# Kernel optimization log

Measured on AMD Instinct MI355X. Metric: run time of the kernel, lower is better.

Reference implementation:

```python
import jax, jax.numpy as jnp
import numpy as np

B, T, D, H = 4, 2048, 1024, 16
DH = D // H

def setup_inputs() -> dict:
    key = jax.random.key(0)
    ks = jax.random.split(key, 8)
    scale = 1.0 / np.sqrt(D)
    return {
        "q": jax.random.normal(ks[0], (B, T, D), dtype=jnp.float32),
        "k": jax.random.normal(ks[1], (B, T, D), dtype=jnp.float32),
        "v": jax.random.normal(ks[2], (B, T, D), dtype=jnp.float32),
        "wq": jax.random.normal(ks[3], (D, D), dtype=jnp.float32) * scale,
        "wk": jax.random.normal(ks[4], (D, D), dtype=jnp.float32) * scale,
        "wv": jax.random.normal(ks[5], (D, D), dtype=jnp.float32) * scale,
        "wo": jax.random.normal(ks[6], (D, D), dtype=jnp.float32) * scale,
        "mask": jnp.tril(jnp.ones((T, T), dtype=bool)),  # causal [Tq,Tk]
    }

def reference(q, k, v, wq, wk, wv, wo, mask):
    Bq, Tq, C = q.shape
    Tk = k.shape[1]
    # nn.Linear(bias=False): y = x @ W.T, W is [out,in]
    qh = (q @ wq.T).reshape(Bq, Tq, H, DH).transpose(0, 2, 1, 3)  # [B,H,Tq,DH]
    kh = (k @ wk.T).reshape(Bq, Tk, H, DH).transpose(0, 2, 1, 3)
    vh = (v @ wv.T).reshape(Bq, Tk, H, DH).transpose(0, 2, 1, 3)
    att = jnp.einsum("bhqd,bhkd->bhqk", qh, kh) / np.sqrt(DH)
    att = jnp.where(mask[None, None, :, :], att, -jnp.inf)
    att = jax.nn.softmax(att, axis=-1)
    out = jnp.einsum("bhqk,bhkd->bhqd", att, vh)
    out = out.transpose(0, 2, 1, 3).reshape(Bq, Tq, C)
    return out @ wo.T
```

## Files before the change

### kernel.cpp

```cpp
#include <hip/hip_runtime.h>
#include <hip/hip_bf16.h>

typedef short bf16x8 __attribute__((ext_vector_type(8)));
typedef float f32x4 __attribute__((ext_vector_type(4)));
typedef float f32x16 __attribute__((ext_vector_type(16)));
typedef unsigned u32x2 __attribute__((ext_vector_type(2)));

#define N_B 4
#define N_T 2048
#define N_D 1024
#define N_H 16
#define N_DH 64

#define Q_SCALE 0.18033688011112042f

__device__ __forceinline__ unsigned short f2bf(float f) {
  union { float f; unsigned int u; } c; c.f = f;
  unsigned int u = c.u;
  return (unsigned short)((u + 0x7FFFu + ((u >> 16) & 1u)) >> 16);
}

__device__ __forceinline__ unsigned cvtpk_bf16(float lo, float hi) {
  unsigned r;
  asm("v_cvt_pk_bf16_f32 %0, %1, %2" : "=v"(r) : "v"(lo), "v"(hi));
  return r;
}

__device__ __forceinline__ void gll16(const unsigned short* g, unsigned short* l) {
  __builtin_amdgcn_global_load_lds(
      (const __attribute__((address_space(1))) unsigned int*)(const void*)g,
      (__attribute__((address_space(3))) unsigned int*)(void*)l, 16, 0, 0);
}

__global__ void cast_w(const float* __restrict__ wq, const float* __restrict__ wk,
                       const float* __restrict__ wv, const float* __restrict__ wo,
                       unsigned short* __restrict__ ws) {
  const int z = blockIdx.z;
  const float* srcs[4] = {wq, wk, wv, wo};
  const float* src = srcs[z];
  unsigned short* d = ws + (size_t)z * (N_D * N_D);
  const int i = (blockIdx.x * 256 + threadIdx.x) * 8;
  float4 a = *(const float4*)(src + i);
  float4 b = *(const float4*)(src + i + 4);
  bf16x8 p;
  p[0] = (short)f2bf(a.x); p[1] = (short)f2bf(a.y);
  p[2] = (short)f2bf(a.z); p[3] = (short)f2bf(a.w);
  p[4] = (short)f2bf(b.x); p[5] = (short)f2bf(b.y);
  p[6] = (short)f2bf(b.z); p[7] = (short)f2bf(b.w);
  *(bf16x8*)(d + i) = p;
}

__launch_bounds__(256, 2)
__global__ void proj_qkv(const float* __restrict__ qf32,
                         const float* __restrict__ kf32,
                         const float* __restrict__ vf32,
                         const unsigned short* __restrict__ wq,
                         const unsigned short* __restrict__ wk,
                         const unsigned short* __restrict__ wv,
                         unsigned short* __restrict__ qh,
                         unsigned short* __restrict__ kh,
                         unsigned short* __restrict__ vt) {
  const int z = blockIdx.z;
  const float* X = (z == 0) ? qf32 : (z == 1) ? kf32 : vf32;
  const unsigned short* W = (z == 0) ? wq : (z == 1) ? wk : wv;
  unsigned short* O = (z == 0) ? qh : (z == 1) ? kh : vt;

  __shared__ unsigned short lds_a[128 * 64];
  __shared__ unsigned short lds_b[128 * 64];

  const int tid = threadIdx.x;
  const int wave = tid >> 6, lane = tid & 63;
  const int wm = wave >> 1, wn = wave & 1;
  const int lr = lane & 15, lg = lane >> 4;
  const int orig = blockIdx.y * 8 + blockIdx.x;
  const int swz = (orig & 7) * 64 + (orig >> 3);
  const int m0 = (swz >> 3) * 128, n0 = (swz & 7) * 128;
  const int sw = (lr & 7) << 4;

  f32x4 acc[4][4] = {};

  for (int k0 = 0; k0 < N_D; k0 += 64) {
    __syncthreads();
#pragma unroll
    for (int it = 0; it < 4; ++it) {
      int c = it * 256 + tid;
      int row = c >> 3;
      int sb = ((c & 7) * 16) ^ ((row & 7) << 4);
      gll16(&W[(size_t)(n0 + row) * N_D + k0 + (sb >> 1)], &lds_b[c * 8]);
    }
#pragma unroll
    for (int it = 0; it < 4; ++it) {
      int c = it * 256 + tid;
      int row = c >> 3;
      int sb = ((c & 7) * 16) ^ ((row & 7) << 4);
      const float* src = &X[(size_t)(m0 + row) * N_D + k0 + (sb >> 1)];
      float4 f0 = ((const float4*)src)[0];
      float4 f1 = ((const float4*)src)[1];
      union { unsigned u[4]; bf16x8 v; } pk;
      pk.u[0] = cvtpk_bf16(f0.x, f0.y); pk.u[1] = cvtpk_bf16(f0.z, f0.w);
      pk.u[2] = cvtpk_bf16(f1.x, f1.y); pk.u[3] = cvtpk_bf16(f1.z, f1.w);
      *(bf16x8*)&lds_a[c * 8] = pk.v;
    }
    __syncthreads();

#pragma unroll
    for (int kk = 0; kk < 2; ++kk) {
      bf16x8 af[4], bfr[4];
      const int cb = (lg * 16 + kk * 64);
#pragma unroll
      for (int m = 0; m < 4; ++m)
        af[m] = *(bf16x8*)&lds_a[(wm * 64 + m * 16 + lr) * 64 + ((cb ^ sw) >> 1)];
#pragma unroll
      for (int n = 0; n < 4; ++n)
        bfr[n] = *(bf16x8*)&lds_b[(wn * 64 + n * 16 + lr) * 64 + ((cb ^ sw) >> 1)];
#pragma unroll
      for (int m = 0; m < 4; ++m)
#pragma unroll
        for (int n = 0; n < 4; ++n)
          acc[m][n] = __builtin_amdgcn_mfma_f32_16x16x32_bf16(af[m], bfr[n], acc[m][n], 0, 0, 0);
    }
  }

  const float osc = (z == 0) ? Q_SCALE : 1.0f;
#pragma unroll
  for (int m = 0; m < 4; ++m)
#pragma unroll
    for (int n = 0; n < 4; ++n)
#pragma unroll
      for (int r = 0; r < 4; ++r) {
        int row = m0 + wm * 64 + m * 16 + lg * 4 + r;
        int col = n0 + wn * 64 + n * 16 + lr;
        int b = row >> 11, t = row & (N_T - 1);
        int hh = col >> 6, dh = col & 63;
        unsigned short val = f2bf(acc[m][n][r] * osc);
        if (z < 2)
          O[(((size_t)(b * N_H + hh)) * N_T + t) * N_DH + dh] = val;
        else
          O[(((size_t)(b * N_H + hh)) * N_DH + dh) * N_T + t] = val;
      }
}

__launch_bounds__(256, 2)
__global__ void proj_out(const unsigned short* __restrict__ A,
                         const unsigned short* __restrict__ W,
                         float* __restrict__ out) {
  __shared__ unsigned short lds_a[128 * 64];
  __shared__ unsigned short lds_b[128 * 64];

  const int tid = threadIdx.x;
  const int wave = tid >> 6, lane = tid & 63;
  const int wm = wave >> 1, wn = wave & 1;
  const int lr = lane & 15, lg = lane >> 4;
  const int orig = blockIdx.y * 8 + blockIdx.x;
  const int swz = (orig & 7) * 64 + (orig >> 3);
  const int m0 = (swz >> 3) * 128, n0 = (swz & 7) * 128;
  const int sw = (lr & 7) << 4;

  f32x4 acc[4][4] = {};

  for (int k0 = 0; k0 < N_D; k0 += 64) {
    __syncthreads();
#pragma unroll
    for (int it = 0; it < 4; ++it) {
      int c = it * 256 + tid;
      int row = c >> 3;
      int sb = ((c & 7) * 16) ^ ((row & 7) << 4);
      gll16(&A[(size_t)(m0 + row) * N_D + k0 + (sb >> 1)], &lds_a[c * 8]);
      gll16(&W[(size_t)(n0 + row) * N_D + k0 + (sb >> 1)], &lds_b[c * 8]);
    }
    __syncthreads();

#pragma unroll
    for (int kk = 0; kk < 2; ++kk) {
      bf16x8 af[4], bfr[4];
      const int cb = (lg * 16 + kk * 64);
#pragma unroll
      for (int m = 0; m < 4; ++m)
        af[m] = *(bf16x8*)&lds_a[(wm * 64 + m * 16 + lr) * 64 + ((cb ^ sw) >> 1)];
#pragma unroll
      for (int n = 0; n < 4; ++n)
        bfr[n] = *(bf16x8*)&lds_b[(wn * 64 + n * 16 + lr) * 64 + ((cb ^ sw) >> 1)];
#pragma unroll
      for (int m = 0; m < 4; ++m)
#pragma unroll
        for (int n = 0; n < 4; ++n)
          acc[m][n] = __builtin_amdgcn_mfma_f32_16x16x32_bf16(af[m], bfr[n], acc[m][n], 0, 0, 0);
    }
  }

#pragma unroll
  for (int m = 0; m < 4; ++m)
#pragma unroll
    for (int n = 0; n < 4; ++n)
#pragma unroll
      for (int r = 0; r < 4; ++r) {
        int row = m0 + wm * 64 + m * 16 + lg * 4 + r;
        int col = n0 + wn * 64 + n * 16 + lr;
        out[(size_t)row * N_D + col] = acc[m][n][r];
      }
}

__launch_bounds__(256, 2)
__global__ void attn(const unsigned short* __restrict__ qh,
                     const unsigned short* __restrict__ kh,
                     const unsigned short* __restrict__ vt,
                     unsigned short* __restrict__ att) {
  __shared__ unsigned short k_lds[2][64 * 64];
  __shared__ unsigned short v_lds[2][64 * 64];

  const int tid = threadIdx.x;
  const int wave = tid >> 6, lane = tid & 63;
  const int l31 = lane & 31, hi = lane >> 5;
  const int L = (int)blockIdx.x + (int)blockIdx.y * 8;
  const int bh = (L & 7) | ((L >> 6) << 3);
  const int px = (L >> 3) & 7;
  const size_t base = (size_t)bh * N_T * N_DH;
  const unsigned short* Q = qh + base;
  const unsigned short* K = kh + base;
  const unsigned short* V = vt + base;
  const int b = bh >> 4, h = bh & 15;
  const int swr = (l31 & 7) << 4;

  bf16x8 ones;
#pragma unroll
  for (int j = 0; j < 8; ++j) ones[j] = (short)0x3F80;

  auto stage = [&](int buf, int kb2) {
    const int kk0 = kb2 * 64;
#pragma unroll
    for (int it = 0; it < 2; ++it) {
      int c = it * 256 + tid;
      int row = c >> 3;
      int sb = ((c & 7) * 16) ^ ((row & 7) << 4);
      gll16(&K[(size_t)(kk0 + row) * N_DH + (sb >> 1)], &k_lds[buf][c * 8]);
      gll16(&V[(size_t)row * N_T + kk0 + (sb >> 1)], &v_lds[buf][c * 8]);
    }
  };

  for (int half = 0; half < 2; ++half) {
    const int qt = half ? (15 - px) : px;
    const int q0w = qt * 128 + wave * 32;

    bf16x8 qf[4];
#pragma unroll
    for (int i = 0; i < 4; ++i)
      qf[i] = *(const bf16x8*)&Q[(size_t)(q0w + l31) * N_DH + i * 16 + hi * 8];

    float m_r = -INFINITY;
    f32x16 l_acc = {};
    f32x16 o0 = {}, o1 = {};

    const int nkb = 2 * qt + 2;

    __syncthreads();
    stage(0, 0);

    for (int kb = 0; kb < nkb; ++kb) {
      const int cur = kb & 1;
      __syncthreads();
      if (kb + 1 < nkb) stage(cur ^ 1, kb + 1);

      const unsigned short* kt_ = k_lds[cur];
      const unsigned short* vt_ = v_lds[cur];

      const int kgb0 = kb * 64;
      const int kgb1 = kb * 64 + 32;
      if (kgb0 > q0w + 31) continue;
      const bool a1 = (kgb1 <= q0w + 31);

      f32x16 s0 = {}, s1 = {};
      __builtin_amdgcn_s_setprio(1);
#pragma unroll
      for (int i = 0; i < 4; ++i) {
        bf16x8 kf = *(const bf16x8*)&kt_[l31 * 64 + (((i * 32 + hi * 16) ^ swr) >> 1)];
        s0 = __builtin_amdgcn_mfma_f32_32x32x16_bf16(kf, qf[i], s0, 0, 0, 0);
      }
      if (a1) {
#pragma unroll
        for (int i = 0; i < 4; ++i) {
          bf16x8 kf = *(const bf16x8*)&kt_[(32 + l31) * 64 + (((i * 32 + hi * 16) ^ swr) >> 1)];
          s1 = __builtin_amdgcn_mfma_f32_32x32x16_bf16(kf, qf[i], s1, 0, 0, 0);
        }
      }
      __builtin_amdgcn_s_setprio(0);

      if (kgb0 == q0w) {
#pragma unroll
        for (int j = 0; j < 16; ++j)
          if ((j & 3) + 8 * (j >> 2) + 4 * hi > l31) s0[j] = -1e30f;
      }
      if (a1 && kgb1 == q0w) {
#pragma unroll
        for (int j = 0; j < 16; ++j)
          if ((j & 3) + 8 * (j >> 2) + 4 * hi > l31) s1[j] = -1e30f;
      }

      float mx = s0[0];
#pragma unroll
      for (int j = 1; j < 16; ++j) mx = fmaxf(mx, s0[j]);
      if (a1) {
#pragma unroll
        for (int j = 0; j < 16; ++j) mx = fmaxf(mx, s1[j]);
      }
      {
        u32x2 rm = __builtin_amdgcn_permlane32_swap(
            __float_as_uint(mx), __float_as_uint(mx), false, false);
        mx = fmaxf(__uint_as_float(rm.x), __uint_as_float(rm.y));
      }
      if (__any(mx > m_r + 8.0f)) {
        float mn = fmaxf(m_r, mx);
        float al = exp2f(m_r - mn);
        m_r = mn;
#pragma unroll
        for (int j = 0; j < 16; ++j) {
          float aj = __shfl(al, (j & 3) + 8 * (j >> 2) + 4 * hi);
          o0[j] *= aj; o1[j] *= aj; l_acc[j] *= aj;
        }
      }

#pragma unroll
      for (int j = 0; j < 16; ++j) s0[j] = exp2f(s0[j] - m_r);
      if (a1) {
#pragma unroll
        for (int j = 0; j < 16; ++j) s1[j] = exp2f(s1[j] - m_r);
      }

      {
        unsigned t01 = cvtpk_bf16(s0[0], s0[1]),   t45 = cvtpk_bf16(s0[4], s0[5]);
        unsigned t23 = cvtpk_bf16(s0[2], s0[3]),   t67 = cvtpk_bf16(s0[6], s0[7]);
        unsigned u01 = cvtpk_bf16(s0[8], s0[9]),   u45 = cvtpk_bf16(s0[12], s0[13]);
        unsigned u23 = cvtpk_bf16(s0[10], s0[11]), u67 = cvtpk_bf16(s0[14], s0[15]);
        u32x2 r0 = __builtin_amdgcn_permlane32_swap(t01, t45, false, false);
        u32x2 r1 = __builtin_amdgcn_permlane32_swap(t23, t67, false, false);
        u32x2 r2 = __builtin_amdgcn_permlane32_swap(u01, u45, false, false);
        u32x2 r3 = __builtin_amdgcn_permlane32_swap(u23, u67, false, false);
        union { unsigned u[4]; bf16x8 v; } pa0, pa1;
        pa0.u[0] = r0.x;  pa0.u[1] = r1.x;  pa0.u[2] = r0.y;  pa0.u[3] = r1.y;
        pa1.u[0] = r2.x;  pa1.u[1] = r3.x;  pa1.u[2] = r2.y;  pa1.u[3] = r3.y;

        const int c0 = ((hi * 16) ^ swr) >> 1;
        const int c1 = ((32 + hi * 16) ^ swr) >> 1;
        bf16x8 v00 = *(const bf16x8*)&vt_[l31 * 64 + c0];
        bf16x8 v01 = *(const bf16x8*)&vt_[(32 + l31) * 64 + c0];
        bf16x8 v10 = *(const bf16x8*)&vt_[l31 * 64 + c1];
        bf16x8 v11 = *(const bf16x8*)&vt_[(32 + l31) * 64 + c1];

        __builtin_amdgcn_s_setprio(1);
        o0 = __builtin_amdgcn_mfma_f32_32x32x16_bf16(pa0.v, v00, o0, 0, 0, 0);
        o1 = __builtin_amdgcn_mfma_f32_32x32x16_bf16(pa0.v, v01, o1, 0, 0, 0);
        o0 = __builtin_amdgcn_mfma_f32_32x32x16_bf16(pa1.v, v10, o0, 0, 0, 0);
        o1 = __builtin_amdgcn_mfma_f32_32x32x16_bf16(pa1.v, v11, o1, 0, 0, 0);
        l_acc = __builtin_amdgcn_mfma_f32_32x32x16_bf16(pa0.v, ones, l_acc, 0, 0, 0);
        l_acc = __builtin_amdgcn_mfma_f32_32x32x16_bf16(pa1.v, ones, l_acc, 0, 0, 0);
        __builtin_amdgcn_s_setprio(0);
      }

      if (a1) {
        unsigned t01 = cvtpk_bf16(s1[0], s1[1]),   t45 = cvtpk_bf16(s1[4], s1[5]);
        unsigned t23 = cvtpk_bf16(s1[2], s1[3]),   t67 = cvtpk_bf16(s1[6], s1[7]);
        unsigned u01 = cvtpk_bf16(s1[8], s1[9]),   u45 = cvtpk_bf16(s1[12], s1[13]);
        unsigned u23 = cvtpk_bf16(s1[10], s1[11]), u67 = cvtpk_bf16(s1[14], s1[15]);
        u32x2 r0 = __builtin_amdgcn_permlane32_swap(t01, t45, false, false);
        u32x2 r1 = __builtin_amdgcn_permlane32_swap(t23, t67, false, false);
        u32x2 r2 = __builtin_amdgcn_permlane32_swap(u01, u45, false, false);
        u32x2 r3 = __builtin_amdgcn_permlane32_swap(u23, u67, false, false);
        union { unsigned u[4]; bf16x8 v; } pb0, pb1;
        pb0.u[0] = r0.x;  pb0.u[1] = r1.x;  pb0.u[2] = r0.y;  pb0.u[3] = r1.y;
        pb1.u[0] = r2.x;  pb1.u[1] = r3.x;  pb1.u[2] = r2.y;  pb1.u[3] = r3.y;

        const int c0 = ((64 + hi * 16) ^ swr) >> 1;
        const int c1 = ((96 + hi * 16) ^ swr) >> 1;
        bf16x8 v00 = *(const bf16x8*)&vt_[l31 * 64 + c0];
        bf16x8 v01 = *(const bf16x8*)&vt_[(32 + l31) * 64 + c0];
        bf16x8 v10 = *(const bf16x8*)&vt_[l31 * 64 + c1];
        bf16x8 v11 = *(const bf16x8*)&vt_[(32 + l31) * 64 + c1];

        __builtin_amdgcn_s_setprio(1);
        o0 = __builtin_amdgcn_mfma_f32_32x32x16_bf16(pb0.v, v00, o0, 0, 0, 0);
        o1 = __builtin_amdgcn_mfma_f32_32x32x16_bf16(pb0.v, v01, o1, 0, 0, 0);
        o0 = __builtin_amdgcn_mfma_f32_32x32x16_bf16(pb1.v, v10, o0, 0, 0, 0);
        o1 = __builtin_amdgcn_mfma_f32_32x32x16_bf16(pb1.v, v11, o1, 0, 0, 0);
        l_acc = __builtin_amdgcn_mfma_f32_32x32x16_bf16(pb0.v, ones, l_acc, 0, 0, 0);
        l_acc = __builtin_amdgcn_mfma_f32_32x32x16_bf16(pb1.v, ones, l_acc, 0, 0, 0);
        __builtin_amdgcn_s_setprio(0);
      }
    }

#pragma unroll
    for (int j = 0; j < 16; ++j) {
      float inv = 1.0f / l_acc[j];
      int t = q0w + (j & 3) + 8 * (j >> 2) + 4 * hi;
      size_t rowb = ((size_t)(b * N_T + t)) * N_D + h * 64 + l31;
      att[rowb]      = f2bf(o0[j] * inv);
      att[rowb + 32] = f2bf(o1[j] * inv);
    }
  }
}

extern "C" void kernel_launch(void* const* d_in, const int* in_sizes, int n_in,
                              void* d_out, int out_size, void* d_ws, size_t ws_size,
                              hipStream_t stream) {
  (void)in_sizes; (void)n_in; (void)out_size; (void)ws_size;
  const float* q  = (const float*)d_in[0];
  const float* k  = (const float*)d_in[1];
  const float* v  = (const float*)d_in[2];
  const float* wq = (const float*)d_in[3];
  const float* wk = (const float*)d_in[4];
  const float* wv = (const float*)d_in[5];
  const float* wo = (const float*)d_in[6];
  float* out = (float*)d_out;

  unsigned short* ws = (unsigned short*)d_ws;
  const size_t W_ELEMS = (size_t)N_D * N_D;
  const size_t T_ELEMS = (size_t)N_B * N_T * N_D;
  unsigned short* wqb = ws;
  unsigned short* wkb = wqb + W_ELEMS;
  unsigned short* wvb = wkb + W_ELEMS;
  unsigned short* wob = wvb + W_ELEMS;
  unsigned short* qhb = wob + W_ELEMS;
  unsigned short* khb = qhb + T_ELEMS;
  unsigned short* vtb = khb + T_ELEMS;
  unsigned short* att = vtb + T_ELEMS;

  cast_w<<<dim3(512, 1, 4), 256, 0, stream>>>(wq, wk, wv, wo, ws);
  proj_qkv<<<dim3(8, 64, 3), 256, 0, stream>>>(q, k, v, wqb, wkb, wvb, qhb, khb, vtb);
  attn<<<dim3(8, N_B * N_H), 256, 0, stream>>>(qhb, khb, vtb, att);
  proj_out<<<dim3(8, 64), 256, 0, stream>>>(att, wob, out);
}
```

Measured before the change: 183.3 us.

## Double-buffer QKV projection LDS tiles and prefetch next K-slice into registers

Adds double-buffered shared-memory tiles for the QKV projection GEMM. The next K-slice of weights is issued into the alternate buffer and the fp32 activations are loaded into registers before the MFMA loop, then converted and written to LDS afterwards. This aims to hide global-load latency behind matrix math and drop one barrier per iteration. In exchange it doubles LDS use to 64KB per block and holds 32 extra VGPRs for the prefetched activations, which may reduce occupancy under the launch bound of 2 blocks.

New measurement: 187.1 us. 1.02x slower.

```diff
diff --git a/kernel.cpp b/kernel.cpp
--- a/kernel.cpp
+++ b/kernel.cpp
@@ -65,8 +65,8 @@
   const unsigned short* W = (z == 0) ? wq : (z == 1) ? wk : wv;
   unsigned short* O = (z == 0) ? qh : (z == 1) ? kh : vt;
 
-  __shared__ unsigned short lds_a[128 * 64];
-  __shared__ unsigned short lds_b[128 * 64];
+  __shared__ unsigned short lds_a[2][128 * 64];
+  __shared__ unsigned short lds_b[2][128 * 64];
 
   const int tid = threadIdx.x;
   const int wave = tid >> 6, lane = tid & 63;
@@ -78,30 +78,53 @@
   const int sw = (lr & 7) << 4;
 
   f32x4 acc[4][4] = {};
-
-  for (int k0 = 0; k0 < N_D; k0 += 64) {
-    __syncthreads();
+  float4 fr[8];
+
+  auto loadB = [&](int buf, int k0) {
 #pragma unroll
     for (int it = 0; it < 4; ++it) {
       int c = it * 256 + tid;
       int row = c >> 3;
       int sb = ((c & 7) * 16) ^ ((row & 7) << 4);
-      gll16(&W[(size_t)(n0 + row) * N_D + k0 + (sb >> 1)], &lds_b[c * 8]);
-    }
+      gll16(&W[(size_t)(n0 + row) * N_D + k0 + (sb >> 1)], &lds_b[buf][c * 8]);
+    }
+  };
+  auto loadA = [&](int k0) {
 #pragma unroll
     for (int it = 0; it < 4; ++it) {
       int c = it * 256 + tid;
       int row = c >> 3;
       int sb = ((c & 7) * 16) ^ ((row & 7) << 4);
       const float* src = &X[(size_t)(m0 + row) * N_D + k0 + (sb >> 1)];
-      float4 f0 = ((const float4*)src)[0];
-      float4 f1 = ((const float4*)src)[1];
+      fr[2 * it]     = ((const float4*)src)[0];
+      fr[2 * it + 1] = ((const float4*)src)[1];
+    }
+  };
+  auto writeA = [&](int buf) {
+#pragma unroll
+    for (int it = 0; it < 4; ++it) {
+      int c = it * 256 + tid;
       union { unsigned u[4]; bf16x8 v; } pk;
-      pk.u[0] = cvtpk_bf16(f0.x, f0.y); pk.u[1] = cvtpk_bf16(f0.z, f0.w);
-      pk.u[2] = cvtpk_bf16(f1.x, f1.y); pk.u[3] = cvtpk_bf16(f1.z, f1.w);
-      *(bf16x8*)&lds_a[c * 8] = pk.v;
-    }
+      pk.u[0] = cvtpk_bf16(fr[2 * it].x, fr[2 * it].y);
+      pk.u[1] = cvtpk_bf16(fr[2 * it].z, fr[2 * it].w);
+      pk.u[2] = cvtpk_bf16(fr[2 * it + 1].x, fr[2 * it + 1].y);
+      pk.u[3] = cvtpk_bf16(fr[2 * it + 1].z, fr[2 * it + 1].w);
+      *(bf16x8*)&lds_a[buf][c * 8] = pk.v;
+    }
+  };
+
+  loadB(0, 0);
+  loadA(0);
+  writeA(0);
+
+  for (int k0 = 0; k0 < N_D; k0 += 64) {
+    const int cur = (k0 >> 6) & 1;
+    const bool more = (k0 + 64 < N_D);
     __syncthreads();
+    if (more) {
+      loadB(cur ^ 1, k0 + 64);
+      loadA(k0 + 64);
+    }
 
 #pragma unroll
     for (int kk = 0; kk < 2; ++kk) {
@@ -109,16 +132,18 @@
       const int cb = (lg * 16 + kk * 64);
 #pragma unroll
       for (int m = 0; m < 4; ++m)
-        af[m] = *(bf16x8*)&lds_a[(wm * 64 + m * 16 + lr) * 64 + ((cb ^ sw) >> 1)];
+        af[m] = *(bf16x8*)&lds_a[cur][(wm * 64 + m * 16 + lr) * 64 + ((cb ^ sw) >> 1)];
 #pragma unroll
       for (int n = 0; n < 4; ++n)
-        bfr[n] = *(bf16x8*)&lds_b[(wn * 64 + n * 16 + lr) * 64 + ((cb ^ sw) >> 1)];
+        bfr[n] = *(bf16x8*)&lds_b[cur][(wn * 64 + n * 16 + lr) * 64 + ((cb ^ sw) >> 1)];
 #pragma unroll
       for (int m = 0; m < 4; ++m)
 #pragma unroll
         for (int n = 0; n < 4; ++n)
           acc[m][n] = __builtin_amdgcn_mfma_f32_16x16x32_bf16(af[m], bfr[n], acc[m][n], 0, 0, 0);
     }
+
+    if (more) writeA(cur ^ 1);
   }
 
   const float osc = (z == 0) ? Q_SCALE : 1.0f;
```
